# Kernel tuning notes

Hardware: AMD Instinct MI355X
Metric: run time of the kernel (lower is better)

The kernel has to match this reference:

```python
import jax, jax.numpy as jnp
import numpy as np

HB, S, DK = 32, 2048, 128  # h*batch, seq_len, d_k
NEG = -1.0e9


def setup_inputs() -> dict:
    key = jax.random.key(0)
    kq, kk, kv = jax.random.split(key, 3)
    Q = jax.random.normal(kq, (HB, S, DK), dtype=jnp.float32)
    K = jax.random.normal(kk, (HB, S, DK), dtype=jnp.float32)
    V = jax.random.normal(kv, (HB, S, DK), dtype=jnp.float32)
    # causal mask, 1.0 where attending allowed, broadcast to all head*batch rows
    mask = jnp.broadcast_to(jnp.tril(jnp.ones((S, S), dtype=jnp.float32)), (HB, S, S))
    return {"Q": Q, "K": K, "V": V, "mask": mask}


def reference(Q, K, V, mask):
    d_k = Q.shape[-1]
    scores = jnp.einsum("bqd,bkd->bqk", Q, K) / jnp.sqrt(jnp.float32(d_k))
    scores = scores * mask + (1.0 - mask) * NEG
    p_attn = jax.nn.softmax(scores, axis=-1)
    # NOTE: original layer computes dropout(p_attn) but then discards it and
    # matmuls the un-dropped p_attn with V; we reproduce the inference math.
    out = jnp.einsum("bqk,bkd->bqd", p_attn, V)
    return (out, p_attn)
```

## Files before the change

kernel.cpp:

```cpp
#include <hip/hip_runtime.h>
#include <hip/hip_bf16.h>
#include <cstdint>

#define HB 32
#define SEQ 2048
#define DKDIM 128

typedef short s16x8 __attribute__((ext_vector_type(8)));
typedef float f32x4 __attribute__((ext_vector_type(4)));

__device__ __forceinline__ unsigned short f2bf(float x) {
  union { float f; uint32_t u; } v; v.f = x;
  uint32_t r = v.u + 0x7FFFu + ((v.u >> 16) & 1u);
  return (unsigned short)(r >> 16);
}
__device__ __forceinline__ float bf2f(unsigned short h) {
  union { uint32_t u; float f; } v; v.u = ((uint32_t)h) << 16;
  return v.f;
}

#define SMEM_BYTES 41088

__global__ __launch_bounds__(256, 3) void attn_fwd_k1(
    const float* __restrict__ Qg, const float* __restrict__ Kg, const float* __restrict__ Vg,
    float* __restrict__ outg, float* __restrict__ pg, float* __restrict__ invlg)
{
  __shared__ __align__(16) unsigned char smem[SMEM_BYTES];
  unsigned short* K_lds  = (unsigned short*)(smem);
  unsigned short* VT_lds = (unsigned short*)(smem + 17408);
  unsigned short* P_lds  = (unsigned short*)(smem + 35840);
  float* rs   = (float*)(smem + 40960);
  float* Ored = (float*)(smem);

  const int tid  = threadIdx.x;
  const int lane = tid & 63;
  const int w    = tid >> 6;
  const int qi   = w >> 1;
  const int ki   = w & 1;
  const int g    = lane >> 4;
  const int lr   = lane & 15;
  const int b    = blockIdx.y;
  const int qt   = blockIdx.x;
  const int qb   = qt << 5;

  if (tid < 32) rs[tid] = 0.0f;

  const float scale = 0.08838834764831845f;

  s16x8 qf[4];
  {
    const float* qrow = Qg + ((size_t)(b * SEQ) + qb + qi * 16 + lr) * DKDIM;
#pragma unroll
    for (int c = 0; c < 4; ++c) {
      const float* p = qrow + c * 32 + g * 8;
      float4 x = *(const float4*)p;
      float4 y = *(const float4*)(p + 4);
      s16x8 h;
      h[0] = (short)f2bf(x.x); h[1] = (short)f2bf(x.y); h[2] = (short)f2bf(x.z); h[3] = (short)f2bf(x.w);
      h[4] = (short)f2bf(y.x); h[5] = (short)f2bf(y.y); h[6] = (short)f2bf(y.z); h[7] = (short)f2bf(y.w);
      qf[c] = h;
    }
  }

  f32x4 oacc[8];
#pragma unroll
  for (int n = 0; n < 8; ++n) { f32x4 z = {0.f, 0.f, 0.f, 0.f}; oacc[n] = z; }
  float rsum[4] = {0.f, 0.f, 0.f, 0.f};

  const int nks   = (qt >> 1) + 1;
  const int qmaxw = qb + qi * 16 + 15;
  const int prow  = lane >> 2;
  const int pc8   = (lane & 3) << 3;

  for (int ks = 0; ks < nks; ++ks) {
    const int kb = ks << 6;
    __syncthreads();
#pragma unroll
    for (int it = 0; it < 4; ++it) {
      int chunk = tid + (it << 8);
      int row = chunk >> 4;
      int c8  = (chunk & 15) << 3;
      const float* src = Kg + ((size_t)(b * SEQ) + kb + row) * DKDIM + c8;
      float4 x = *(const float4*)src;
      float4 y = *(const float4*)(src + 4);
      s16x8 h;
      h[0] = (short)f2bf(x.x); h[1] = (short)f2bf(x.y); h[2] = (short)f2bf(x.z); h[3] = (short)f2bf(x.w);
      h[4] = (short)f2bf(y.x); h[5] = (short)f2bf(y.y); h[6] = (short)f2bf(y.z); h[7] = (short)f2bf(y.w);
      *(s16x8*)(&K_lds[row * 136 + c8]) = h;
    }
    {
      int row = tid & 63;
#pragma unroll
      for (int it = 0; it < 4; ++it) {
        int c8 = (((tid >> 6) + (it << 2))) << 3;
        const float* src = Vg + ((size_t)(b * SEQ) + kb + row) * DKDIM + c8;
        float4 x = *(const float4*)src;
        float4 y = *(const float4*)(src + 4);
        float vv[8] = {x.x, x.y, x.z, x.w, y.x, y.y, y.z, y.w};
#pragma unroll
        for (int i = 0; i < 8; ++i) VT_lds[(c8 + i) * 72 + row] = f2bf(vv[i]);
      }
    }
    __syncthreads();

    const int kw = kb + (ki << 5);
    const bool active = (kw <= qmaxw);
    if (active) {
      f32x4 sacc[2];
      { f32x4 z = {0.f, 0.f, 0.f, 0.f}; sacc[0] = z; sacc[1] = z; }
#pragma unroll
      for (int kk = 0; kk < 2; ++kk) {
#pragma unroll
        for (int c = 0; c < 4; ++c) {
          s16x8 bf = *(const s16x8*)(&K_lds[((ki << 5) + (kk << 4) + lr) * 136 + (c << 5) + (g << 3)]);
          sacc[kk] = __builtin_amdgcn_mfma_f32_16x16x32_bf16(qf[c], bf, sacc[kk], 0, 0, 0);
        }
      }
#pragma unroll
      for (int kk = 0; kk < 2; ++kk) {
        const int colg = kw + (kk << 4) + lr;
#pragma unroll
        for (int r = 0; r < 4; ++r) {
          const int rowq = qb + qi * 16 + (g << 2) + r;
          float e = (colg <= rowq) ? __expf(sacc[kk][r] * scale) : 0.0f;
          rsum[r] += e;
          P_lds[w * 640 + ((g << 2) + r) * 40 + (kk << 4) + lr] = f2bf(e);
        }
      }
    }
    __syncthreads();
    {
      float* dst = pg + ((size_t)(b * SEQ) + qb + qi * 16 + prow) * SEQ + kw + pc8;
      if (active) {
        s16x8 ph = *(const s16x8*)(&P_lds[w * 640 + prow * 40 + pc8]);
        float4 o0, o1;
        o0.x = bf2f((unsigned short)ph[0]); o0.y = bf2f((unsigned short)ph[1]);
        o0.z = bf2f((unsigned short)ph[2]); o0.w = bf2f((unsigned short)ph[3]);
        o1.x = bf2f((unsigned short)ph[4]); o1.y = bf2f((unsigned short)ph[5]);
        o1.z = bf2f((unsigned short)ph[6]); o1.w = bf2f((unsigned short)ph[7]);
        *(float4*)dst = o0;
        *(float4*)(dst + 4) = o1;
        s16x8 pa = *(const s16x8*)(&P_lds[w * 640 + lr * 40 + (g << 3)]);
#pragma unroll
        for (int n = 0; n < 8; ++n) {
          s16x8 vb = *(const s16x8*)(&VT_lds[(n * 16 + lr) * 72 + (ki << 5) + (g << 3)]);
          oacc[n] = __builtin_amdgcn_mfma_f32_16x16x32_bf16(pa, vb, oacc[n], 0, 0, 0);
        }
      } else {
        float4 z; z.x = z.y = z.z = z.w = 0.f;
        *(float4*)dst = z;
        *(float4*)(dst + 4) = z;
      }
    }
  }

#pragma unroll
  for (int r = 0; r < 4; ++r) {
    float v = rsum[r];
    v += __shfl_xor(v, 1, 64);
    v += __shfl_xor(v, 2, 64);
    v += __shfl_xor(v, 4, 64);
    v += __shfl_xor(v, 8, 64);
    rsum[r] = v;
  }
  __syncthreads();
  if (lr == 0) {
#pragma unroll
    for (int r = 0; r < 4; ++r) atomicAdd(&rs[qi * 16 + (g << 2) + r], rsum[r]);
  }
  __syncthreads();
  if (tid < 32) invlg[(size_t)(b * SEQ) + qb + tid] = 1.0f / rs[tid];

  if (ki == 1) {
#pragma unroll
    for (int n = 0; n < 8; ++n)
#pragma unroll
      for (int r = 0; r < 4; ++r)
        Ored[(qi * 16 + (g << 2) + r) * 128 + n * 16 + lr] = oacc[n][r];
  }
  __syncthreads();
  if (ki == 0) {
#pragma unroll
    for (int n = 0; n < 8; ++n) {
#pragma unroll
      for (int r = 0; r < 4; ++r) {
        const int rq = qi * 16 + (g << 2) + r;
        const float inv = 1.0f / rs[rq];
        float val = (oacc[n][r] + Ored[rq * 128 + n * 16 + lr]) * inv;
        outg[((size_t)(b * SEQ) + qb + rq) * DKDIM + n * 16 + lr] = val;
      }
    }
  }
}

__global__ __launch_bounds__(256) void attn_fwd_k2(float* __restrict__ pg, const float* __restrict__ invlg) {
  const size_t total = (size_t)HB * SEQ * (SEQ / 4);
  size_t i4 = (size_t)blockIdx.x * blockDim.x + threadIdx.x;
  const size_t stride = (size_t)gridDim.x * blockDim.x;
  for (; i4 < total; i4 += stride) {
    const size_t rowid = i4 >> 9;
    const int q  = (int)(rowid & (SEQ - 1));
    const int k0 = ((int)(i4 & 511)) << 2;
    const int kcov = (q & ~63) + 64;
    float4* p = (float4*)pg + i4;
    if (k0 < kcov) {
      const float s = invlg[rowid];
      float4 v = *p;
      v.x *= s; v.y *= s; v.z *= s; v.w *= s;
      *p = v;
    } else {
      float4 z; z.x = z.y = z.z = z.w = 0.f;
      *p = z;
    }
  }
}

extern "C" void kernel_launch(void* const* d_in, const int* in_sizes, int n_in,
                              void* d_out, int out_size, void* d_ws, size_t ws_size,
                              hipStream_t stream) {
  const float* Q = (const float*)d_in[0];
  const float* K = (const float*)d_in[1];
  const float* V = (const float*)d_in[2];
  float* out  = (float*)d_out;
  float* p    = out + (size_t)HB * SEQ * DKDIM;
  float* invl = (float*)d_ws;

  dim3 grid1(SEQ / 32, HB);
  attn_fwd_k1<<<grid1, 256, 0, stream>>>(Q, K, V, out, p, invl);
  attn_fwd_k2<<<8192, 256, 0, stream>>>(p, invl);
}
```

Before: 1.278 ms.

## Fuse softmax normalization into a two-pass single attention kernel

Result: slower. 1.650 ms (+29.2%).

```diff
diff --git a/kernel.cpp b/kernel.cpp
--- a/kernel.cpp
+++ b/kernel.cpp
@@ -5,6 +5,9 @@
 #define HB 32
 #define SEQ 2048
 #define DKDIM 128
+#define KPAD 140
+#define VPAD 76
+#define PPAD 76
 
 typedef short s16x8 __attribute__((ext_vector_type(8)));
 typedef float f32x4 __attribute__((ext_vector_type(4)));
@@ -19,141 +22,115 @@
   return v.f;
 }
 
-#define SMEM_BYTES 41088
-
-__global__ __launch_bounds__(256, 3) void attn_fwd_k1(
+#define K_BYTES  (64 * KPAD * 2)
+#define VT_BYTES (128 * VPAD * 2)
+#define P_BYTES  (4 * 16 * PPAD * 2)
+#define SMEM_BYTES (K_BYTES + VT_BYTES + P_BYTES)
+
+__global__ __launch_bounds__(256, 3) void attn_fwd(
     const float* __restrict__ Qg, const float* __restrict__ Kg, const float* __restrict__ Vg,
-    float* __restrict__ outg, float* __restrict__ pg, float* __restrict__ invlg)
+    float* __restrict__ outg, float* __restrict__ pg)
 {
   __shared__ __align__(16) unsigned char smem[SMEM_BYTES];
   unsigned short* K_lds  = (unsigned short*)(smem);
-  unsigned short* VT_lds = (unsigned short*)(smem + 17408);
-  unsigned short* P_lds  = (unsigned short*)(smem + 35840);
-  float* rs   = (float*)(smem + 40960);
-  float* Ored = (float*)(smem);
+  unsigned short* VT_lds = (unsigned short*)(smem + K_BYTES);
+  unsigned short* P_lds  = (unsigned short*)(smem + K_BYTES + VT_BYTES);
 
   const int tid  = threadIdx.x;
   const int lane = tid & 63;
   const int w    = tid >> 6;
-  const int qi   = w >> 1;
-  const int ki   = w & 1;
   const int g    = lane >> 4;
   const int lr   = lane & 15;
   const int b    = blockIdx.y;
-  const int qt   = blockIdx.x;
-  const int qb   = qt << 5;
-
-  if (tid < 32) rs[tid] = 0.0f;
+  const int x    = blockIdx.x;
+  const int qt   = (x & 1) ? (31 - (x >> 1)) : (x >> 1);
+  const int qb   = qt << 6;
+  const size_t bS = (size_t)b * SEQ;
+  const int nks  = qt + 1;
 
   const float scale = 0.08838834764831845f;
-
   s16x8 qf[4];
   {
-    const float* qrow = Qg + ((size_t)(b * SEQ) + qb + qi * 16 + lr) * DKDIM;
+    const float* qrow = Qg + (bS + qb + w * 16 + lr) * DKDIM;
 #pragma unroll
     for (int c = 0; c < 4; ++c) {
       const float* p = qrow + c * 32 + g * 8;
-      float4 x = *(const float4*)p;
-      float4 y = *(const float4*)(p + 4);
+      float4 a = *(const float4*)p;
+      float4 bb = *(const float4*)(p + 4);
       s16x8 h;
-      h[0] = (short)f2bf(x.x); h[1] = (short)f2bf(x.y); h[2] = (short)f2bf(x.z); h[3] = (short)f2bf(x.w);
-      h[4] = (short)f2bf(y.x); h[5] = (short)f2bf(y.y); h[6] = (short)f2bf(y.z); h[7] = (short)f2bf(y.w);
+      h[0] = (short)f2bf(a.x * scale); h[1] = (short)f2bf(a.y * scale);
+      h[2] = (short)f2bf(a.z * scale); h[3] = (short)f2bf(a.w * scale);
+      h[4] = (short)f2bf(bb.x * scale); h[5] = (short)f2bf(bb.y * scale);
+      h[6] = (short)f2bf(bb.z * scale); h[7] = (short)f2bf(bb.w * scale);
       qf[c] = h;
     }
   }
 
-  f32x4 oacc[8];
-#pragma unroll
-  for (int n = 0; n < 8; ++n) { f32x4 z = {0.f, 0.f, 0.f, 0.f}; oacc[n] = z; }
-  float rsum[4] = {0.f, 0.f, 0.f, 0.f};
-
-  const int nks   = (qt >> 1) + 1;
-  const int qmaxw = qb + qi * 16 + 15;
-  const int prow  = lane >> 2;
-  const int pc8   = (lane & 3) << 3;
-
-  for (int ks = 0; ks < nks; ++ks) {
-    const int kb = ks << 6;
-    __syncthreads();
+  auto stageK = [&](unsigned short* dst, int kb) {
 #pragma unroll
     for (int it = 0; it < 4; ++it) {
       int chunk = tid + (it << 8);
       int row = chunk >> 4;
       int c8  = (chunk & 15) << 3;
-      const float* src = Kg + ((size_t)(b * SEQ) + kb + row) * DKDIM + c8;
-      float4 x = *(const float4*)src;
-      float4 y = *(const float4*)(src + 4);
+      const float* src = Kg + (bS + kb + row) * DKDIM + c8;
+      float4 a = *(const float4*)src;
+      float4 bb = *(const float4*)(src + 4);
       s16x8 h;
-      h[0] = (short)f2bf(x.x); h[1] = (short)f2bf(x.y); h[2] = (short)f2bf(x.z); h[3] = (short)f2bf(x.w);
-      h[4] = (short)f2bf(y.x); h[5] = (short)f2bf(y.y); h[6] = (short)f2bf(y.z); h[7] = (short)f2bf(y.w);
-      *(s16x8*)(&K_lds[row * 136 + c8]) = h;
-    }
-    {
-      int row = tid & 63;
-#pragma unroll
-      for (int it = 0; it < 4; ++it) {
-        int c8 = (((tid >> 6) + (it << 2))) << 3;
-        const float* src = Vg + ((size_t)(b * SEQ) + kb + row) * DKDIM + c8;
-        float4 x = *(const float4*)src;
-        float4 y = *(const float4*)(src + 4);
-        float vv[8] = {x.x, x.y, x.z, x.w, y.x, y.y, y.z, y.w};
-#pragma unroll
-        for (int i = 0; i < 8; ++i) VT_lds[(c8 + i) * 72 + row] = f2bf(vv[i]);
+      h[0] = (short)f2bf(a.x); h[1] = (short)f2bf(a.y); h[2] = (short)f2bf(a.z); h[3] = (short)f2bf(a.w);
+      h[4] = (short)f2bf(bb.x); h[5] = (short)f2bf(bb.y); h[6] = (short)f2bf(bb.z); h[7] = (short)f2bf(bb.w);
+      *(s16x8*)(&dst[row * KPAD + c8]) = h;
+    }
+  };
+  auto stageV = [&](int kb) {
+    int row = tid & 63;
+#pragma unroll
+    for (int it = 0; it < 4; ++it) {
+      int c8 = (((tid >> 6) + (it << 2))) << 3;
+      const float* src = Vg + (bS + kb + row) * DKDIM + c8;
+      float4 a = *(const float4*)src;
+      float4 bb = *(const float4*)(src + 4);
+      float vv[8] = {a.x, a.y, a.z, a.w, bb.x, bb.y, bb.z, bb.w};
+#pragma unroll
+      for (int i = 0; i < 8; ++i) VT_lds[(c8 + i) * VPAD + row] = f2bf(vv[i]);
+    }
+  };
+
+  float rsum[4] = {0.f, 0.f, 0.f, 0.f};
+  unsigned short* bufs[2] = {K_lds, VT_lds};
+
+  stageK(bufs[0], 0);
+  for (int ks = 0; ks < nks; ++ks) {
+    __syncthreads();
+    if (ks + 1 < nks) stageK(bufs[(ks + 1) & 1], (ks + 1) << 6);
+    const unsigned short* kb_lds = bufs[ks & 1];
+    f32x4 sacc[4];
+#pragma unroll
+    for (int n = 0; n < 4; ++n) { f32x4 z = {0.f, 0.f, 0.f, 0.f}; sacc[n] = z; }
+#pragma unroll
+    for (int c = 0; c < 4; ++c) {
+#pragma unroll
+      for (int n = 0; n < 4; ++n) {
+        s16x8 bf = *(const s16x8*)(&kb_lds[(n * 16 + lr) * KPAD + (c << 5) + (g << 3)]);
+        sacc[n] = __builtin_amdgcn_mfma_f32_16x16x32_bf16(qf[c], bf, sacc[n], 0, 0, 0);
       }
     }
-    __syncthreads();
-
-    const int kw = kb + (ki << 5);
-    const bool active = (kw <= qmaxw);
-    if (active) {
-      f32x4 sacc[2];
-      { f32x4 z = {0.f, 0.f, 0.f, 0.f}; sacc[0] = z; sacc[1] = z; }
-#pragma unroll
-      for (int kk = 0; kk < 2; ++kk) {
-#pragma unroll
-        for (int c = 0; c < 4; ++c) {
-          s16x8 bf = *(const s16x8*)(&K_lds[((ki << 5) + (kk << 4) + lr) * 136 + (c << 5) + (g << 3)]);
-          sacc[kk] = __builtin_amdgcn_mfma_f32_16x16x32_bf16(qf[c], bf, sacc[kk], 0, 0, 0);
+    if (ks == qt) {
+#pragma unroll
+      for (int n = 0; n < 4; ++n)
+#pragma unroll
+        for (int r = 0; r < 4; ++r) {
+          const bool ok = (n * 16 + lr) <= (w * 16 + g * 4 + r);
+          rsum[r] += ok ? __expf(sacc[n][r]) : 0.0f;
         }
-      }
-#pragma unroll
-      for (int kk = 0; kk < 2; ++kk) {
-        const int colg = kw + (kk << 4) + lr;
-#pragma unroll
-        for (int r = 0; r < 4; ++r) {
-          const int rowq = qb + qi * 16 + (g << 2) + r;
-          float e = (colg <= rowq) ? __expf(sacc[kk][r] * scale) : 0.0f;
-          rsum[r] += e;
-          P_lds[w * 640 + ((g << 2) + r) * 40 + (kk << 4) + lr] = f2bf(e);
-        }
-      }
-    }
-    __syncthreads();
-    {
-      float* dst = pg + ((size_t)(b * SEQ) + qb + qi * 16 + prow) * SEQ + kw + pc8;
-      if (active) {
-        s16x8 ph = *(const s16x8*)(&P_lds[w * 640 + prow * 40 + pc8]);
-        float4 o0, o1;
-        o0.x = bf2f((unsigned short)ph[0]); o0.y = bf2f((unsigned short)ph[1]);
-        o0.z = bf2f((unsigned short)ph[2]); o0.w = bf2f((unsigned short)ph[3]);
-        o1.x = bf2f((unsigned short)ph[4]); o1.y = bf2f((unsigned short)ph[5]);
-        o1.z = bf2f((unsigned short)ph[6]); o1.w = bf2f((unsigned short)ph[7]);
-        *(float4*)dst = o0;
-        *(float4*)(dst + 4) = o1;
-        s16x8 pa = *(const s16x8*)(&P_lds[w * 640 + lr * 40 + (g << 3)]);
-#pragma unroll
-        for (int n = 0; n < 8; ++n) {
-          s16x8 vb = *(const s16x8*)(&VT_lds[(n * 16 + lr) * 72 + (ki << 5) + (g << 3)]);
-          oacc[n] = __builtin_amdgcn_mfma_f32_16x16x32_bf16(pa, vb, oacc[n], 0, 0, 0);
-        }
-      } else {
-        float4 z; z.x = z.y = z.z = z.w = 0.f;
-        *(float4*)dst = z;
-        *(float4*)(dst + 4) = z;
-      }
-    }
-  }
-
+    } else {
+#pragma unroll
+      for (int n = 0; n < 4; ++n)
+#pragma unroll
+        for (int r = 0; r < 4; ++r) rsum[r] += __expf(sacc[n][r]);
+    }
+  }
+
+  float inv[4];
 #pragma unroll
   for (int r = 0; r < 4; ++r) {
     float v = rsum[r];
@@ -161,56 +138,99 @@
     v += __shfl_xor(v, 2, 64);
     v += __shfl_xor(v, 4, 64);
     v += __shfl_xor(v, 8, 64);
-    rsum[r] = v;
-  }
-  __syncthreads();
-  if (lr == 0) {
-#pragma unroll
-    for (int r = 0; r < 4; ++r) atomicAdd(&rs[qi * 16 + (g << 2) + r], rsum[r]);
-  }
-  __syncthreads();
-  if (tid < 32) invlg[(size_t)(b * SEQ) + qb + tid] = 1.0f / rs[tid];
-
-  if (ki == 1) {
-#pragma unroll
-    for (int n = 0; n < 8; ++n)
-#pragma unroll
-      for (int r = 0; r < 4; ++r)
-        Ored[(qi * 16 + (g << 2) + r) * 128 + n * 16 + lr] = oacc[n][r];
-  }
-  __syncthreads();
-  if (ki == 0) {
-#pragma unroll
-    for (int n = 0; n < 8; ++n) {
-#pragma unroll
-      for (int r = 0; r < 4; ++r) {
-        const int rq = qi * 16 + (g << 2) + r;
-        const float inv = 1.0f / rs[rq];
-        float val = (oacc[n][r] + Ored[rq * 128 + n * 16 + lr]) * inv;
-        outg[((size_t)(b * SEQ) + qb + rq) * DKDIM + n * 16 + lr] = val;
+    inv[r] = 1.0f / v;
+  }
+
+  f32x4 oacc[8];
+#pragma unroll
+  for (int n = 0; n < 8; ++n) { f32x4 z = {0.f, 0.f, 0.f, 0.f}; oacc[n] = z; }
+  unsigned short* Pw = P_lds + w * 16 * PPAD;
+  const int prow = lane >> 2;
+  const int pc16 = (lane & 3) << 4;
+
+  for (int ks = 0; ks < nks; ++ks) {
+    const int kb = ks << 6;
+    __syncthreads();
+    stageK(K_lds, kb);
+    stageV(kb);
+    __syncthreads();
+
+    f32x4 sacc[4];
+#pragma unroll
+    for (int n = 0; n < 4; ++n) { f32x4 z = {0.f, 0.f, 0.f, 0.f}; sacc[n] = z; }
+#pragma unroll
+    for (int c = 0; c < 4; ++c) {
+#pragma unroll
+      for (int n = 0; n < 4; ++n) {
+        s16x8 bf = *(const s16x8*)(&K_lds[(n * 16 + lr) * KPAD + (c << 5) + (g << 3)]);
+        sacc[n] = __builtin_amdgcn_mfma_f32_16x16x32_bf16(qf[c], bf, sacc[n], 0, 0, 0);
       }
     }
-  }
-}
-
-__global__ __launch_bounds__(256) void attn_fwd_k2(float* __restrict__ pg, const float* __restrict__ invlg) {
-  const size_t total = (size_t)HB * SEQ * (SEQ / 4);
-  size_t i4 = (size_t)blockIdx.x * blockDim.x + threadIdx.x;
-  const size_t stride = (size_t)gridDim.x * blockDim.x;
-  for (; i4 < total; i4 += stride) {
-    const size_t rowid = i4 >> 9;
-    const int q  = (int)(rowid & (SEQ - 1));
-    const int k0 = ((int)(i4 & 511)) << 2;
-    const int kcov = (q & ~63) + 64;
-    float4* p = (float4*)pg + i4;
-    if (k0 < kcov) {
-      const float s = invlg[rowid];
-      float4 v = *p;
-      v.x *= s; v.y *= s; v.z *= s; v.w *= s;
-      *p = v;
+    if (ks == qt) {
+#pragma unroll
+      for (int n = 0; n < 4; ++n)
+#pragma unroll
+        for (int r = 0; r < 4; ++r) {
+          const bool ok = (n * 16 + lr) <= (w * 16 + g * 4 + r);
+          float e = ok ? __expf(sacc[n][r]) * inv[r] : 0.0f;
+          Pw[(g * 4 + r) * PPAD + n * 16 + lr] = f2bf(e);
+        }
     } else {
-      float4 z; z.x = z.y = z.z = z.w = 0.f;
-      *p = z;
+#pragma unroll
+      for (int n = 0; n < 4; ++n)
+#pragma unroll
+        for (int r = 0; r < 4; ++r) {
+          float e = __expf(sacc[n][r]) * inv[r];
+          Pw[(g * 4 + r) * PPAD + n * 16 + lr] = f2bf(e);
+        }
+    }
+    asm volatile("s_waitcnt lgkmcnt(0)" ::: "memory");
+
+    {
+      float* dst = pg + (bS + qb + w * 16 + prow) * SEQ + kb + pc16;
+      s16x8 p0 = *(const s16x8*)(&Pw[prow * PPAD + pc16]);
+      s16x8 p1 = *(const s16x8*)(&Pw[prow * PPAD + pc16 + 8]);
+      float4 o;
+      o.x = bf2f((unsigned short)p0[0]); o.y = bf2f((unsigned short)p0[1]);
+      o.z = bf2f((unsigned short)p0[2]); o.w = bf2f((unsigned short)p0[3]);
+      *(float4*)dst = o;
+      o.x = bf2f((unsigned short)p0[4]); o.y = bf2f((unsigned short)p0[5]);
+      o.z = bf2f((unsigned short)p0[6]); o.w = bf2f((unsigned short)p0[7]);
+      *(float4*)(dst + 4) = o;
+      o.x = bf2f((unsigned short)p1[0]); o.y = bf2f((unsigned short)p1[1]);
+      o.z = bf2f((unsigned short)p1[2]); o.w = bf2f((unsigned short)p1[3]);
+      *(float4*)(dst + 8) = o;
+      o.x = bf2f((unsigned short)p1[4]); o.y = bf2f((unsigned short)p1[5]);
+      o.z = bf2f((unsigned short)p1[6]); o.w = bf2f((unsigned short)p1[7]);
+      *(float4*)(dst + 12) = o;
+    }
+#pragma unroll
+    for (int kk = 0; kk < 2; ++kk) {
+      s16x8 pa = *(const s16x8*)(&Pw[lr * PPAD + (kk << 5) + (g << 3)]);
+#pragma unroll
+      for (int n = 0; n < 8; ++n) {
+        s16x8 vb = *(const s16x8*)(&VT_lds[(n * 16 + lr) * VPAD + (kk << 5) + (g << 3)]);
+        oacc[n] = __builtin_amdgcn_mfma_f32_16x16x32_bf16(pa, vb, oacc[n], 0, 0, 0);
+      }
+    }
+  }
+
+#pragma unroll
+  for (int n = 0; n < 8; ++n)
+#pragma unroll
+    for (int r = 0; r < 4; ++r)
+      outg[(bS + qb + w * 16 + g * 4 + r) * DKDIM + n * 16 + lr] = oacc[n][r];
+
+  const int kcov = nks << 6;
+  if (kcov < SEQ) {
+    f32x4 z = {0.f, 0.f, 0.f, 0.f};
+    const int r0 = tid >> 4;
+    const int cl = (tid & 15) << 2;
+#pragma unroll
+    for (int rr = r0; rr < 64; rr += 16) {
+      float* prow_ = pg + (bS + qb + rr) * SEQ;
+      for (int c = kcov + cl; c < SEQ; c += 64)
+        *(f32x4*)(prow_ + c) = z;
     }
   }
 }
@@ -221,11 +241,9 @@
   const float* Q = (const float*)d_in[0];
   const float* K = (const float*)d_in[1];
   const float* V = (const float*)d_in[2];
-  float* out  = (float*)d_out;
-  float* p    = out + (size_t)HB * SEQ * DKDIM;
-  float* invl = (float*)d_ws;
-
-  dim3 grid1(SEQ / 32, HB);
-  attn_fwd_k1<<<grid1, 256, 0, stream>>>(Q, K, V, out, p, invl);
-  attn_fwd_k2<<<8192, 256, 0, stream>>>(p, invl);
-}
+  float* out = (float*)d_out;
+  float* p   = out + (size_t)HB * SEQ * DKDIM;
+
+  dim3 grid(SEQ / 64, HB);
+  attn_fwd<<<grid, 256, 0, stream>>>(Q, K, V, out, p);
+}
```
